# Optimization experiments

Measured on AMD Instinct MI355X. Metric: run time of the kernel, lower is better.

The kernel has to match this reference:

```python
import jax, jax.numpy as jnp
import numpy as np

D = 256      # model_dim
H = 4        # num_heads
DPH = D // H # dim_per_head = 64
NLBL = 9     # number of per-label linear layers


def setup_inputs() -> dict:
    key0 = jax.random.key(0)
    ks = jax.random.split(key0, 16)
    N, M = 6144, 6144
    s = 1.0 / np.sqrt(D)
    inp = {
        'key':     jax.random.normal(ks[0], (N, D), jnp.float32),
        'value':   jax.random.normal(ks[1], (N, D), jnp.float32),
        'query':   jax.random.normal(ks[2], (M, D), jnp.float32),
        'label_1': jax.random.randint(ks[3], (N,), 0, NLBL),
        'label_2': jax.random.randint(ks[4], (M,), 0, NLBL),
        # 9 per-label projection weights (applied as x @ W + b)
        'Wq': jax.random.normal(ks[5], (NLBL, D, D), jnp.float32) * s,
        'bq': jax.random.normal(ks[6], (NLBL, D), jnp.float32) * 0.02,
        'Wk': jax.random.normal(ks[7], (NLBL, D, D), jnp.float32) * s,
        'bk': jax.random.normal(ks[8], (NLBL, D), jnp.float32) * 0.02,
        'Wv': jax.random.normal(ks[9], (NLBL, D, D), jnp.float32) * s,
        'bv': jax.random.normal(ks[10], (NLBL, D), jnp.float32) * 0.02,
        'Wf': jax.random.normal(ks[11], (D, D), jnp.float32) * s,
        'bf': jax.random.normal(ks[12], (D,), jnp.float32) * 0.02,
        'gamma': jnp.ones((D,), jnp.float32),
        'beta':  jnp.zeros((D,), jnp.float32),
    }
    return inp


def _label_proj(x, W, b, lbl):
    # Project every token with all 9 label weights, then pick the per-token one.
    # p: [n, 9, D]
    p = jnp.einsum('nd,ldo->nlo', x, W) + b[None]
    return jnp.take_along_axis(p, lbl[:, None, None], axis=1)[:, 0]  # [n, D]


def reference(key, value, query, label_1, label_2,
              Wq, bq, Wk, bk, Wv, bv, Wf, bf, gamma, beta):
    M = query.shape[0]
    # Per-label (dynamically routed) projections; within a group the query
    # label equals the key label, so per-token weight selection is exactly
    # the per-group loop of the original module.
    q = _label_proj(query, Wq, bq, label_2).reshape(M, H, DPH)
    k = _label_proj(key,   Wk, bk, label_1).reshape(-1, H, DPH)
    v = _label_proj(value, Wv, bv, label_1).reshape(-1, H, DPH)

    # Note: original uses scale = (dim_per_head // num_heads) ** -0.5
    scale = (DPH // H) ** (-0.5)
    scores = jnp.einsum('mhd,nhd->hmn', q, k) * scale  # [H, M, N]

    # Queries only attend to keys of the same label (block structure of
    # the original per-label gather/attention/scatter loop).
    mask = label_2[:, None] == label_1[None, :]        # [M, N]
    probs = jax.nn.softmax(jnp.where(mask[None], scores, -1e30), axis=-1)

    ctx = jnp.einsum('hmn,nhd->mhd', probs, v).reshape(M, D)
    out = ctx @ Wf + bf
    res = query + out  # residual is the unprojected query

    mu = jnp.mean(res, axis=-1, keepdims=True)
    var = jnp.var(res, axis=-1, keepdims=True)
    return (res - mu) / jnp.sqrt(var + 1e-5) * gamma + beta
```

## Files before the change

kernel.cpp:

```cpp
#include <hip/hip_runtime.h>
#include <hip/hip_bf16.h>

#define D 256
#define H 4
#define DPH 64
#define NLBL 9
#define SPLITK 4

typedef __attribute__((ext_vector_type(8))) __bf16 bf16x8;
typedef __attribute__((ext_vector_type(8))) unsigned short u16x8;
typedef __attribute__((ext_vector_type(4))) float f32x4;

__device__ __forceinline__ int sw_idx(int row, int col) {
  return row * 64 + (col ^ ((row & 7) << 3));
}

__device__ __forceinline__ unsigned int pk2(float a, float b) {
  unsigned int lo = (unsigned int)__builtin_bit_cast(unsigned short, (__bf16)a);
  unsigned int hi = (unsigned int)__builtin_bit_cast(unsigned short, (__bf16)b);
  return lo | (hi << 16);
}

__device__ __forceinline__ bf16x8 cvt8(float4 u0, float4 u1) {
  bf16x8 r;
  r[0] = (__bf16)u0.x; r[1] = (__bf16)u0.y; r[2] = (__bf16)u0.z; r[3] = (__bf16)u0.w;
  r[4] = (__bf16)u1.x; r[5] = (__bf16)u1.y; r[6] = (__bf16)u1.z; r[7] = (__bf16)u1.w;
  return r;
}

__global__ __launch_bounds__(1024) void hist_kernel(
    const int* __restrict__ lbl1, int n1, const int* __restrict__ lbl2, int n2,
    int* __restrict__ cnt) {
  const int a = blockIdx.x;
  const int n = (a == 0) ? n1 : n2;
  const int* lbl = (a == 0) ? lbl1 : lbl2;
  const int t = threadIdx.x, lane = t & 63;

  __shared__ int bins[NLBL];
  if (t < NLBL) bins[t] = 0;
  __syncthreads();

  for (int chunk = 0; chunk < n; chunk += 1024) {
    int i = chunk + t;
    int l = (i < n) ? lbl[i] : -1;
#pragma unroll
    for (int lab = 0; lab < NLBL; ++lab) {
      unsigned long long bal = __ballot(l == lab);
      if (lane == 0 && bal) atomicAdd(&bins[lab], __popcll(bal));
    }
  }
  __syncthreads();
  if (t < NLBL) cnt[a * NLBL + t] = bins[t];
}

__global__ void offsets_kernel(const int* __restrict__ cnt, int* __restrict__ off,
                               int* __restrict__ pqo, int* __restrict__ pko,
                               int* __restrict__ tq, int* __restrict__ tk,
                               int* __restrict__ ntl) {
  if (threadIdx.x != 0) return;
  int a0 = 0, a1 = 0, p0 = 0, p1 = 0, t0 = 0, t1 = 0;
  for (int l = 0; l < NLBL; ++l) {
    off[l] = a0;      a0 += cnt[l];
    off[10 + l] = a1; a1 += cnt[NLBL + l];
    pko[l] = p0; pqo[l] = p1;
    int tkl = (cnt[l] + 63) >> 6, tql = (cnt[NLBL + l] + 63) >> 6;
    for (int i = 0; i < tkl; ++i) { tk[2 * t0] = l; tk[2 * t0 + 1] = p0 + (i << 6); ++t0; }
    for (int i = 0; i < tql; ++i) { tq[2 * t1] = l; tq[2 * t1 + 1] = p1 + (i << 6); ++t1; }
    p0 += tkl << 6; p1 += tql << 6;
  }
  off[9] = a0; off[19] = a1; pko[9] = p0; pqo[9] = p1;
  ntl[0] = t1; ntl[1] = t0;
}

__global__ __launch_bounds__(1024) void scatter_kernel(
    const int* __restrict__ lbl1, int n1, const int* __restrict__ lbl2, int n2,
    const int* __restrict__ off, int* __restrict__ korder, int* __restrict__ qorder) {
  const int l = blockIdx.x;
  const int a = blockIdx.y;
  const int n = (a == 0) ? n1 : n2;
  const int* lbl = (a == 0) ? lbl1 : lbl2;
  int* order = (a == 0) ? korder : qorder;
  const int base = off[a * 10 + l];

  const int t = threadIdx.x, wave = t >> 6, lane = t & 63;
  __shared__ int wtot[16];
  int pos = 0;
  for (int chunk = 0; chunk < n; chunk += 1024) {
    int i = chunk + t;
    bool flag = (i < n) && (lbl[i] == l);
    unsigned long long bal = __ballot(flag);
    int wprefix = __popcll(bal & ((1ull << lane) - 1ull));
    if (lane == 0) wtot[wave] = __popcll(bal);
    __syncthreads();
    int prew = 0, tot = 0;
#pragma unroll
    for (int w = 0; w < 16; ++w) {
      prew += (w < wave) ? wtot[w] : 0;
      tot += wtot[w];
    }
    if (flag) order[base + pos + prew + wprefix] = i;
    pos += tot;
    __syncthreads();
  }
}

__global__ __launch_bounds__(256) void transW_kernel(
    const float* __restrict__ Wq, const float* __restrict__ Wk,
    const float* __restrict__ Wv, const float* __restrict__ Wf,
    __bf16* __restrict__ Wqt, __bf16* __restrict__ Wkt,
    __bf16* __restrict__ Wvt, __bf16* __restrict__ Wft) {
  int m = blockIdx.y, sub = blockIdx.x;
  const float* src; __bf16* dst;
  if (m < 9)       { src = Wq + (size_t)m * 65536;        dst = Wqt + (size_t)m * 65536; }
  else if (m < 18) { src = Wk + (size_t)(m - 9) * 65536;  dst = Wkt + (size_t)(m - 9) * 65536; }
  else if (m < 27) { src = Wv + (size_t)(m - 18) * 65536; dst = Wvt + (size_t)(m - 18) * 65536; }
  else             { src = Wf;                            dst = Wft; }
  int k0 = (sub >> 2) << 6, n0 = (sub & 3) << 6;
  __shared__ float lds[64][65];
  int t = threadIdx.x, rr = t >> 6, c = t & 63;
#pragma unroll
  for (int i = 0; i < 16; ++i) {
    int r = i * 4 + rr;
    lds[r][c] = src[(size_t)(k0 + r) * D + n0 + c];
  }
  __syncthreads();
#pragma unroll
  for (int i = 0; i < 16; ++i) {
    int r = i * 4 + rr;
    dst[(size_t)(n0 + r) * D + k0 + c] = (__bf16)lds[c][r];
  }
}

__global__ __launch_bounds__(256) void gemm_in_kernel(
    const float* __restrict__ query, const float* __restrict__ key,
    const float* __restrict__ value,
    const __bf16* __restrict__ Wqt, const __bf16* __restrict__ Wkt,
    const __bf16* __restrict__ Wvt,
    const float* __restrict__ bq, const float* __restrict__ bk,
    const float* __restrict__ bv,
    const int* __restrict__ qorder, const int* __restrict__ korder,
    const int* __restrict__ off, const int* __restrict__ cnt,
    const int* __restrict__ pqo, const int* __restrict__ pko,
    const int* __restrict__ tq, const int* __restrict__ tk,
    const int* __restrict__ ntl,
    __bf16* __restrict__ qbuf, __bf16* __restrict__ kbuf, __bf16* __restrict__ vbuf) {
  const int y = blockIdx.y;
  const int nt = (y == 0) ? ntl[0] : ntl[1];
  const int ti = blockIdx.x >> 1, half = blockIdx.x & 1;
  if (ti >= nt) return;
  const int* tt = (y == 0) ? tq : tk;
  const float* x = (y == 0) ? query : (y == 1 ? key : value);
  const __bf16* W = (y == 0) ? Wqt : (y == 1 ? Wkt : Wvt);
  const float* bias = (y == 0) ? bq : (y == 1 ? bk : bv);
  const int* order = (y == 0) ? qorder : korder;
  const int* po = (y == 0) ? pqo : pko;
  __bf16* outp = (y == 0) ? qbuf : (y == 1 ? kbuf : vbuf);
  const float sc = (y == 0) ? 0.36067376f : 1.0f;

  const int l = tt[2 * ti], prow0 = tt[2 * ti + 1] + half * 32;
  const int cl = (y == 0) ? cnt[NLBL + l] : cnt[l];
  const int ooff = (y == 0) ? off[10 + l] : off[l];
  const int base = prow0 - po[l];

  const int t = threadIdx.x, w = t >> 6, lane = t & 63;
  const int lr = lane & 15, lk = lane >> 4;

  int src[2];
#pragma unroll
  for (int fi = 0; fi < 2; ++fi) {
    int ridx = base + fi * 16 + lr;
    src[fi] = (ridx < cl) ? order[ooff + ridx] : -1;
  }

  bf16x8 az;
#pragma unroll
  for (int j = 0; j < 8; ++j) az[j] = (__bf16)0.f;

  f32x4 acc[2][4];
#pragma unroll
  for (int i = 0; i < 2; ++i)
#pragma unroll
    for (int j = 0; j < 4; ++j) acc[i][j] = (f32x4){0.f, 0.f, 0.f, 0.f};

  for (int kb = 0; kb < 8; ++kb) {
    const int kbase = kb * 32 + lk * 8;
    bf16x8 a[2], b[4];
#pragma unroll
    for (int fi = 0; fi < 2; ++fi) {
      if (src[fi] >= 0) {
        const float* ap = x + (size_t)src[fi] * D + kbase;
        float4 u0 = *(const float4*)ap;
        float4 u1 = *(const float4*)(ap + 4);
        a[fi] = cvt8(u0, u1);
      } else {
        a[fi] = az;
      }
    }
#pragma unroll
    for (int fj = 0; fj < 4; ++fj) {
      int col = w * 64 + fj * 16 + lr;
      b[fj] = *(const bf16x8*)(W + (size_t)l * 65536 + (size_t)col * D + kbase);
    }
#pragma unroll
    for (int fi = 0; fi < 2; ++fi)
#pragma unroll
      for (int fj = 0; fj < 4; ++fj)
        acc[fi][fj] = __builtin_amdgcn_mfma_f32_16x16x32_bf16(a[fi], b[fj], acc[fi][fj], 0, 0, 0);
  }

#pragma unroll
  for (int fj = 0; fj < 4; ++fj) {
    int col = w * 64 + fj * 16 + lr;
    float bv_ = bias[l * D + col];
#pragma unroll
    for (int fi = 0; fi < 2; ++fi)
#pragma unroll
      for (int r = 0; r < 4; ++r) {
        int row = prow0 + fi * 16 + lk * 4 + r;
        outp[(size_t)row * D + col] = (__bf16)((acc[fi][fj][r] + bv_) * sc);
      }
  }
}

__global__ __launch_bounds__(256) void attn_mfma(
    const __bf16* __restrict__ qbuf, const __bf16* __restrict__ kbuf,
    const __bf16* __restrict__ vbuf, const int* __restrict__ cnt,
    const int* __restrict__ tq, const int* __restrict__ ntl,
    const int* __restrict__ pko,
    float* __restrict__ pctx, float* __restrict__ pstats) {
  const int tqi = blockIdx.x;
  if (tqi >= ntl[0]) return;
  const int l = tq[2 * tqi], prow0 = tq[2 * tqi + 1];
  const int h = blockIdx.y, s = blockIdx.z;
  const int nk = cnt[l];
  const int ntiles = (nk + 63) >> 6;
  const int ntsz = (ntiles + SPLITK - 1) / SPLITK;
  const int tt0 = s * ntsz;
  const int tt1 = min(ntiles, tt0 + ntsz);
  if (tt0 >= tt1) return;

  const int t = threadIdx.x;
  const int w = t >> 6, lane = t & 63;
  const int lr = lane & 15, lk = lane >> 4;

  __shared__ __align__(16) unsigned short ks[4096];
  __shared__ __align__(16) unsigned short vtl[4096];
  __shared__ __align__(16) unsigned short plds[4096];

  const int qloc = w * 16 + lr;
  const int qrow = prow0 + qloc;
  bf16x8 b_q[2];
#pragma unroll
  for (int kb = 0; kb < 2; ++kb)
    b_q[kb] = *(const bf16x8*)(qbuf + (size_t)qrow * D + h * DPH + kb * 32 + lk * 8);

  f32x4 acc_o[4];
#pragma unroll
  for (int i = 0; i < 4; ++i) acc_o[i] = (f32x4){0.f, 0.f, 0.f, 0.f};
  float mrun = -3.4e38f, lrun = 0.f;
  const int kb0 = pko[l];

  for (int tt = tt0; tt < tt1; ++tt) {
    const int n0 = tt << 6;
    __syncthreads();
    {
      int row = t >> 2, c0 = (t & 3) * 16;
      const uint4* kp = (const uint4*)(kbuf + (size_t)(kb0 + n0 + row) * D + h * DPH + c0);
      uint4 k0 = kp[0], k1 = kp[1];
      *(uint4*)&ks[sw_idx(row, c0)] = k0;
      *(uint4*)&ks[sw_idx(row, c0 + 8)] = k1;
    }
    {
      int key2 = (t & 31) * 2, d0 = (t >> 5) * 8;
      const unsigned short* vp = (const unsigned short*)(vbuf + (size_t)(kb0 + n0 + key2) * D + h * DPH + d0);
      u16x8 va = *(const u16x8*)vp;
      u16x8 vb = *(const u16x8*)(vp + D);
#pragma unroll
      for (int j = 0; j < 8; ++j) {
        unsigned int u = (unsigned int)va[j] | ((unsigned int)vb[j] << 16);
        *(unsigned int*)&vtl[sw_idx(d0 + j, key2)] = u;
      }
    }
    __syncthreads();

    f32x4 s_acc[4];
    const f32x4 zz = {0.f, 0.f, 0.f, 0.f};
#pragma unroll
    for (int fi = 0; fi < 4; ++fi) {
      bf16x8 a0 = *(const bf16x8*)&ks[sw_idx(fi * 16 + lr, lk * 8)];
      s_acc[fi] = __builtin_amdgcn_mfma_f32_16x16x32_bf16(a0, b_q[0], zz, 0, 0, 0);
    }
#pragma unroll
    for (int fi = 0; fi < 4; ++fi) {
      bf16x8 a1 = *(const bf16x8*)&ks[sw_idx(fi * 16 + lr, 32 + lk * 8)];
      s_acc[fi] = __builtin_amdgcn_mfma_f32_16x16x32_bf16(a1, b_q[1], s_acc[fi], 0, 0, 0);
    }

    float p[16];
    float tm = -3.4e38f;
#pragma unroll
    for (int fi = 0; fi < 4; ++fi)
#pragma unroll
      for (int r = 0; r < 4; ++r) {
        int key = n0 + fi * 16 + lk * 4 + r;
        float v = (key < nk) ? s_acc[fi][r] : -1e30f;
        p[fi * 4 + r] = v;
        tm = fmaxf(tm, v);
      }
    tm = fmaxf(tm, __shfl_xor(tm, 16, 64));
    tm = fmaxf(tm, __shfl_xor(tm, 32, 64));
    float mnew = fmaxf(mrun, tm);
    float alpha = exp2f(mrun - mnew);
    lrun *= alpha;
#pragma unroll
    for (int fi = 0; fi < 4; ++fi) acc_o[fi] = acc_o[fi] * alpha;
    float ts = 0.f;
#pragma unroll
    for (int i = 0; i < 16; ++i) { p[i] = exp2f(p[i] - mnew); ts += p[i]; }
    ts += __shfl_xor(ts, 16, 64);
    ts += __shfl_xor(ts, 32, 64);
    lrun += ts;
    mrun = mnew;

#pragma unroll
    for (int fi = 0; fi < 4; ++fi) {
      unsigned int w0 = pk2(p[fi * 4 + 0], p[fi * 4 + 1]);
      unsigned int w1 = pk2(p[fi * 4 + 2], p[fi * 4 + 3]);
      int idx = w * 1024 + sw_idx(lr, fi * 16 + lk * 4);
      *(uint2*)&plds[idx] = make_uint2(w0, w1);
    }

#pragma unroll
    for (int kb = 0; kb < 2; ++kb) {
      bf16x8 bp = *(const bf16x8*)&plds[w * 1024 + sw_idx(lr, kb * 32 + lk * 8)];
#pragma unroll
      for (int fi = 0; fi < 4; ++fi) {
        bf16x8 av = *(const bf16x8*)&vtl[sw_idx(fi * 16 + lr, kb * 32 + lk * 8)];
        acc_o[fi] = __builtin_amdgcn_mfma_f32_16x16x32_bf16(av, bp, acc_o[fi], 0, 0, 0);
      }
    }
  }

  const size_t base = ((size_t)tqi * H + h) * SPLITK + s;
  float* pc = pctx + base * 4096;
#pragma unroll
  for (int fi = 0; fi < 4; ++fi)
    *(f32x4*)(pc + qloc * 64 + fi * 16 + lk * 4) = acc_o[fi];
  if (lk == 0) {
    pstats[base * 128 + qloc * 2] = mrun;
    pstats[base * 128 + qloc * 2 + 1] = lrun;
  }
}

__global__ __launch_bounds__(256) void attn_reduce(
    const float* __restrict__ pctx, const float* __restrict__ pstats,
    const int* __restrict__ cnt, const int* __restrict__ tq,
    const int* __restrict__ ntl, __bf16* __restrict__ cg) {
  const int tqi = blockIdx.x;
  if (tqi >= ntl[0]) return;
  const int l = tq[2 * tqi], prow0 = tq[2 * tqi + 1];
  const int h = blockIdx.y;
  const int t = threadIdx.x;
  const int q = t >> 2, part = t & 3;

  __bf16* op = cg + (size_t)(prow0 + q) * D + h * DPH + part * 16;

  const int nk = cnt[l];
  const int ntiles = (nk + 63) >> 6;
  float o[16];
#pragma unroll
  for (int j = 0; j < 16; ++j) o[j] = 0.f;

  if (ntiles > 0) {
    const int ntsz = (ntiles + SPLITK - 1) / SPLITK;
    const int nsp = (ntiles + ntsz - 1) / ntsz;
    const size_t base0 = ((size_t)tqi * H + h) * SPLITK;

    float m = -3.4e38f;
    for (int s = 0; s < nsp; ++s)
      m = fmaxf(m, pstats[(base0 + s) * 128 + q * 2]);
    float L = 0.f;
    float wgt[SPLITK];
    for (int s = 0; s < nsp; ++s) {
      float ms = pstats[(base0 + s) * 128 + q * 2];
      float ls = pstats[(base0 + s) * 128 + q * 2 + 1];
      wgt[s] = exp2f(ms - m);
      L += ls * wgt[s];
    }
    float inv = (L > 0.f) ? (1.f / L) : 0.f;
    for (int s = 0; s < nsp; ++s) {
      const float* pc = pctx + (base0 + s) * 4096 + q * 64 + part * 16;
      float wg = wgt[s] * inv;
#pragma unroll
      for (int j = 0; j < 16; ++j) o[j] += pc[j] * wg;
    }
  }

  uint4 o0, o1;
  o0.x = pk2(o[0], o[1]);  o0.y = pk2(o[2], o[3]);
  o0.z = pk2(o[4], o[5]);  o0.w = pk2(o[6], o[7]);
  o1.x = pk2(o[8], o[9]);  o1.y = pk2(o[10], o[11]);
  o1.z = pk2(o[12], o[13]); o1.w = pk2(o[14], o[15]);
  *(uint4*)op = o0;
  *(uint4*)(op + 8) = o1;
}

__global__ __launch_bounds__(256) void proj_ln_kernel(
    const __bf16* __restrict__ cg, const __bf16* __restrict__ Wft,
    const float* __restrict__ bf_, const float* __restrict__ query,
    const int* __restrict__ qorder, const int* __restrict__ off,
    const int* __restrict__ cnt, const int* __restrict__ pqo,
    const int* __restrict__ tq, const int* __restrict__ ntl,
    const float* __restrict__ gamma, const float* __restrict__ beta,
    float* __restrict__ out) {
  const int tqi = blockIdx.x;
  if (tqi >= ntl[0]) return;
  const int l = tq[2 * tqi];
  const int prow0 = tq[2 * tqi + 1] + blockIdx.y * 32;
  const int cl = cnt[NLBL + l];
  const int ooff = off[10 + l];
  const int base = prow0 - pqo[l];

  const int t = threadIdx.x, w = t >> 6, lane = t & 63;
  const int lr = lane & 15, lk = lane >> 4;

  __shared__ int srcs[32];
  __shared__ float psum[4][32], psum2[4][32];
  __shared__ float mu_s[32], is_s[32];

  if (t < 32) {
    int ridx = base + t;
    srcs[t] = (ridx < cl) ? qorder[ooff + ridx] : -1;
  }

  f32x4 acc[2][4];
#pragma unroll
  for (int i = 0; i < 2; ++i)
#pragma unroll
    for (int j = 0; j < 4; ++j) acc[i][j] = (f32x4){0.f, 0.f, 0.f, 0.f};

  for (int kb = 0; kb < 8; ++kb) {
    const int kbase = kb * 32 + lk * 8;
    bf16x8 a[2], b[4];
#pragma unroll
    for (int fi = 0; fi < 2; ++fi)
      a[fi] = *(const bf16x8*)(cg + (size_t)(prow0 + fi * 16 + lr) * D + kbase);
#pragma unroll
    for (int fj = 0; fj < 4; ++fj) {
      int col = w * 64 + fj * 16 + lr;
      b[fj] = *(const bf16x8*)(Wft + (size_t)col * D + kbase);
    }
#pragma unroll
    for (int fi = 0; fi < 2; ++fi)
#pragma unroll
      for (int fj = 0; fj < 4; ++fj)
        acc[fi][fj] = __builtin_amdgcn_mfma_f32_16x16x32_bf16(a[fi], b[fj], acc[fi][fj], 0, 0, 0);
  }

  __syncthreads();

  float res[2][4][4];
  float s1[2][4], s2[2][4];
#pragma unroll
  for (int fi = 0; fi < 2; ++fi)
#pragma unroll
    for (int r = 0; r < 4; ++r) { s1[fi][r] = 0.f; s2[fi][r] = 0.f; }

#pragma unroll
  for (int fj = 0; fj < 4; ++fj) {
    int col = w * 64 + fj * 16 + lr;
    float bcol = bf_[col];
#pragma unroll
    for (int fi = 0; fi < 2; ++fi)
#pragma unroll
      for (int r = 0; r < 4; ++r) {
        int rowl = fi * 16 + lk * 4 + r;
        int sr = srcs[rowl];
        float qv = (sr >= 0) ? query[(size_t)sr * D + col] : 0.f;
        float v = acc[fi][fj][r] + bcol + qv;
        res[fi][fj][r] = v;
        s1[fi][r] += v;
        s2[fi][r] += v * v;
      }
  }

#pragma unroll
  for (int o2 = 1; o2 <= 8; o2 <<= 1) {
#pragma unroll
    for (int fi = 0; fi < 2; ++fi)
#pragma unroll
      for (int r = 0; r < 4; ++r) {
        s1[fi][r] += __shfl_xor(s1[fi][r], o2, 64);
        s2[fi][r] += __shfl_xor(s2[fi][r], o2, 64);
      }
  }
  if (lr == 0) {
#pragma unroll
    for (int fi = 0; fi < 2; ++fi)
#pragma unroll
      for (int r = 0; r < 4; ++r) {
        int rowl = fi * 16 + lk * 4 + r;
        psum[w][rowl] = s1[fi][r];
        psum2[w][rowl] = s2[fi][r];
      }
  }
  __syncthreads();
  if (t < 32) {
    float tot = psum[0][t] + psum[1][t] + psum[2][t] + psum[3][t];
    float tot2 = psum2[0][t] + psum2[1][t] + psum2[2][t] + psum2[3][t];
    float mu = tot * (1.f / D);
    float var = tot2 * (1.f / D) - mu * mu;
    mu_s[t] = mu;
    is_s[t] = rsqrtf(var + 1e-5f);
  }
  __syncthreads();

#pragma unroll
  for (int fj = 0; fj < 4; ++fj) {
    int col = w * 64 + fj * 16 + lr;
    float gc = gamma[col], bc = beta[col];
#pragma unroll
    for (int fi = 0; fi < 2; ++fi)
#pragma unroll
      for (int r = 0; r < 4; ++r) {
        int rowl = fi * 16 + lk * 4 + r;
        int sr = srcs[rowl];
        if (sr >= 0)
          out[(size_t)sr * D + col] =
              (res[fi][fj][r] - mu_s[rowl]) * is_s[rowl] * gc + bc;
      }
  }
}

extern "C" void kernel_launch(void* const* d_in, const int* in_sizes, int n_in,
                              void* d_out, int out_size, void* d_ws, size_t ws_size,
                              hipStream_t stream) {
  const float* key   = (const float*)d_in[0];
  const float* value = (const float*)d_in[1];
  const float* query = (const float*)d_in[2];
  const int*   lbl1  = (const int*)d_in[3];
  const int*   lbl2  = (const int*)d_in[4];
  const float* Wq = (const float*)d_in[5];
  const float* bq = (const float*)d_in[6];
  const float* Wk = (const float*)d_in[7];
  const float* bk = (const float*)d_in[8];
  const float* Wv = (const float*)d_in[9];
  const float* bv = (const float*)d_in[10];
  const float* Wf = (const float*)d_in[11];
  const float* bf_ = (const float*)d_in[12];
  const float* gamma = (const float*)d_in[13];
  const float* beta  = (const float*)d_in[14];
  float* out = (float*)d_out;

  const int N = in_sizes[0] / D;
  const int M = in_sizes[2] / D;
  const int MP = M + NLBL * 64;
  const int NP = N + NLBL * 64;
  const int TQCAP = (M + 63) / 64 + NLBL;
  const int TKCAP = (N + 63) / 64 + NLBL;

  int* cnt = (int*)d_ws;
  int* off = cnt + 32;
  int* pqo = off + 32;
  int* pko = pqo + 16;
  int* ntl = pko + 16;
  int* tq  = ntl + 16;
  int* tk  = tq + 2 * TQCAP;
  int* korder = tk + 2 * TKCAP;
  int* qorder = korder + N;
  size_t ihdr = (((size_t)(112 + 2 * TQCAP + 2 * TKCAP + N + M)) * 4 + 255) & ~(size_t)255;

  __bf16* Wqt = (__bf16*)((char*)d_ws + ihdr);
  __bf16* Wkt = Wqt + (size_t)9 * 65536;
  __bf16* Wvt = Wkt + (size_t)9 * 65536;
  __bf16* Wft = Wvt + (size_t)9 * 65536;
  __bf16* cg  = Wft + 65536;
  __bf16* qbuf = cg + (size_t)MP * D;
  __bf16* kbuf = qbuf + (size_t)MP * D;
  __bf16* vbuf = kbuf + (size_t)NP * D;
  float* pctx = (float*)(vbuf + (size_t)NP * D);
  float* pstats = pctx + (size_t)TQCAP * H * SPLITK * 4096;

  hist_kernel<<<2, 1024, 0, stream>>>(lbl1, N, lbl2, M, cnt);
  offsets_kernel<<<1, 1, 0, stream>>>(cnt, off, pqo, pko, tq, tk, ntl);
  dim3 sgrid(NLBL, 2);
  scatter_kernel<<<sgrid, 1024, 0, stream>>>(lbl1, N, lbl2, M, off, korder, qorder);

  transW_kernel<<<dim3(16, 28), 256, 0, stream>>>(Wq, Wk, Wv, Wf, Wqt, Wkt, Wvt, Wft);

  int gx = (TQCAP > TKCAP) ? TQCAP : TKCAP;
  gemm_in_kernel<<<dim3(gx * 2, 3), 256, 0, stream>>>(
      query, key, value, Wqt, Wkt, Wvt, bq, bk, bv,
      qorder, korder, off, cnt, pqo, pko, tq, tk, ntl, qbuf, kbuf, vbuf);

  attn_mfma<<<dim3(TQCAP, H, SPLITK), 256, 0, stream>>>(
      qbuf, kbuf, vbuf, cnt, tq, ntl, pko, pctx, pstats);

  attn_reduce<<<dim3(TQCAP, H), 256, 0, stream>>>(pctx, pstats, cnt, tq, ntl, cg);

  proj_ln_kernel<<<dim3(TQCAP, 2), 256, 0, stream>>>(
      cg, Wft, bf_, query, qorder, off, cnt, pqo, tq, ntl, gamma, beta, out);
}
```

Baseline: 104.9 us.

## Enlarge query tiles, drop running max, fuse split-K reduce into projection

Merges the histogram and offsets kernels into one single-block setup kernel. Query tiles grow to 128 rows so each attention wave processes two 16-row query fragments per K/V tile, doubling K/V reuse from LDS. The online-softmax running max and rescaling are removed and probabilities use exp2 of the raw scaled scores directly. The separate split-K reduce kernel is folded into proj_ln, which sums the partial contexts into LDS before the output GEMM. Skipping the max subtraction risks overflow for large scores, and the larger tiles reduce grid parallelism.

```diff
diff --git a/kernel.cpp b/kernel.cpp
--- a/kernel.cpp
+++ b/kernel.cpp
@@ -28,48 +28,45 @@
   return r;
 }
 
-__global__ __launch_bounds__(1024) void hist_kernel(
+__global__ __launch_bounds__(1024) void setup_kernel(
     const int* __restrict__ lbl1, int n1, const int* __restrict__ lbl2, int n2,
-    int* __restrict__ cnt) {
-  const int a = blockIdx.x;
-  const int n = (a == 0) ? n1 : n2;
-  const int* lbl = (a == 0) ? lbl1 : lbl2;
+    int* __restrict__ cnt, int* __restrict__ off,
+    int* __restrict__ pqo, int* __restrict__ pko,
+    int* __restrict__ tq, int* __restrict__ tk, int* __restrict__ ntl) {
   const int t = threadIdx.x, lane = t & 63;
-
-  __shared__ int bins[NLBL];
-  if (t < NLBL) bins[t] = 0;
-  __syncthreads();
-
-  for (int chunk = 0; chunk < n; chunk += 1024) {
-    int i = chunk + t;
-    int l = (i < n) ? lbl[i] : -1;
-#pragma unroll
-    for (int lab = 0; lab < NLBL; ++lab) {
-      unsigned long long bal = __ballot(l == lab);
-      if (lane == 0 && bal) atomicAdd(&bins[lab], __popcll(bal));
-    }
-  }
-  __syncthreads();
-  if (t < NLBL) cnt[a * NLBL + t] = bins[t];
-}
-
-__global__ void offsets_kernel(const int* __restrict__ cnt, int* __restrict__ off,
-                               int* __restrict__ pqo, int* __restrict__ pko,
-                               int* __restrict__ tq, int* __restrict__ tk,
-                               int* __restrict__ ntl) {
-  if (threadIdx.x != 0) return;
-  int a0 = 0, a1 = 0, p0 = 0, p1 = 0, t0 = 0, t1 = 0;
-  for (int l = 0; l < NLBL; ++l) {
-    off[l] = a0;      a0 += cnt[l];
-    off[10 + l] = a1; a1 += cnt[NLBL + l];
-    pko[l] = p0; pqo[l] = p1;
-    int tkl = (cnt[l] + 63) >> 6, tql = (cnt[NLBL + l] + 63) >> 6;
-    for (int i = 0; i < tkl; ++i) { tk[2 * t0] = l; tk[2 * t0 + 1] = p0 + (i << 6); ++t0; }
-    for (int i = 0; i < tql; ++i) { tq[2 * t1] = l; tq[2 * t1 + 1] = p1 + (i << 6); ++t1; }
-    p0 += tkl << 6; p1 += tql << 6;
-  }
-  off[9] = a0; off[19] = a1; pko[9] = p0; pqo[9] = p1;
-  ntl[0] = t1; ntl[1] = t0;
+  __shared__ int bins[2 * NLBL];
+  if (t < 2 * NLBL) bins[t] = 0;
+  __syncthreads();
+  for (int a = 0; a < 2; ++a) {
+    const int n = a ? n2 : n1;
+    const int* lbl = a ? lbl2 : lbl1;
+    for (int chunk = 0; chunk < n; chunk += 1024) {
+      int i = chunk + t;
+      int l = (i < n) ? lbl[i] : -1;
+#pragma unroll
+      for (int lab = 0; lab < NLBL; ++lab) {
+        unsigned long long bal = __ballot(l == lab);
+        if (lane == 0 && bal) atomicAdd(&bins[a * NLBL + lab], __popcll(bal));
+      }
+    }
+  }
+  __syncthreads();
+  if (t < 2 * NLBL) cnt[t] = bins[t];
+  if (t == 0) {
+    int a0 = 0, a1 = 0, p0 = 0, p1 = 0, t0 = 0, t1 = 0;
+    for (int l = 0; l < NLBL; ++l) {
+      off[l] = a0;      a0 += bins[l];
+      off[10 + l] = a1; a1 += bins[NLBL + l];
+      pko[l] = p0; pqo[l] = p1;
+      int tkl = (bins[l] + 63) >> 6;
+      int tql = (bins[NLBL + l] + 127) >> 7;
+      for (int i = 0; i < tkl; ++i) { tk[2 * t0] = l; tk[2 * t0 + 1] = p0 + (i << 6); ++t0; }
+      for (int i = 0; i < tql; ++i) { tq[2 * t1] = l; tq[2 * t1 + 1] = p1 + (i << 7); ++t1; }
+      p0 += tkl << 6; p1 += tql << 7;
+    }
+    off[9] = a0; off[19] = a1; pko[9] = p0; pqo[9] = p1;
+    ntl[0] = t1; ntl[1] = t0;
+  }
 }
 
 __global__ __launch_bounds__(1024) void scatter_kernel(
@@ -146,7 +143,8 @@
     __bf16* __restrict__ qbuf, __bf16* __restrict__ kbuf, __bf16* __restrict__ vbuf) {
   const int y = blockIdx.y;
   const int nt = (y == 0) ? ntl[0] : ntl[1];
-  const int ti = blockIdx.x >> 1, half = blockIdx.x & 1;
+  const int ti = (y == 0) ? ((int)blockIdx.x >> 2) : ((int)blockIdx.x >> 1);
+  const int sub = (y == 0) ? ((int)blockIdx.x & 3) : ((int)blockIdx.x & 1);
   if (ti >= nt) return;
   const int* tt = (y == 0) ? tq : tk;
   const float* x = (y == 0) ? query : (y == 1 ? key : value);
@@ -157,7 +155,7 @@
   __bf16* outp = (y == 0) ? qbuf : (y == 1 ? kbuf : vbuf);
   const float sc = (y == 0) ? 0.36067376f : 1.0f;
 
-  const int l = tt[2 * ti], prow0 = tt[2 * ti + 1] + half * 32;
+  const int l = tt[2 * ti], prow0 = tt[2 * ti + 1] + sub * 32;
   const int cl = (y == 0) ? cnt[NLBL + l] : cnt[l];
   const int ooff = (y == 0) ? off[10 + l] : off[l];
   const int base = prow0 - po[l];
@@ -245,19 +243,23 @@
 
   __shared__ __align__(16) unsigned short ks[4096];
   __shared__ __align__(16) unsigned short vtl[4096];
-  __shared__ __align__(16) unsigned short plds[4096];
-
-  const int qloc = w * 16 + lr;
-  const int qrow = prow0 + qloc;
-  bf16x8 b_q[2];
-#pragma unroll
-  for (int kb = 0; kb < 2; ++kb)
-    b_q[kb] = *(const bf16x8*)(qbuf + (size_t)qrow * D + h * DPH + kb * 32 + lk * 8);
-
-  f32x4 acc_o[4];
-#pragma unroll
-  for (int i = 0; i < 4; ++i) acc_o[i] = (f32x4){0.f, 0.f, 0.f, 0.f};
-  float mrun = -3.4e38f, lrun = 0.f;
+  __shared__ __align__(16) unsigned short plds[8192];
+
+  const int qbase = prow0 + w * 32;
+  bf16x8 b_q[2][2];
+#pragma unroll
+  for (int qf = 0; qf < 2; ++qf)
+#pragma unroll
+    for (int kb = 0; kb < 2; ++kb)
+      b_q[qf][kb] = *(const bf16x8*)(qbuf + (size_t)(qbase + qf * 16 + lr) * D +
+                                     h * DPH + kb * 32 + lk * 8);
+
+  f32x4 acc_o[2][4];
+#pragma unroll
+  for (int qf = 0; qf < 2; ++qf)
+#pragma unroll
+    for (int i = 0; i < 4; ++i) acc_o[qf][i] = (f32x4){0.f, 0.f, 0.f, 0.f};
+  float lrun[2] = {0.f, 0.f};
   const int kb0 = pko[l];
 
   for (int tt = tt0; tt < tt1; ++tt) {
@@ -283,131 +285,83 @@
     }
     __syncthreads();
 
-    f32x4 s_acc[4];
+    f32x4 s_acc[2][4];
     const f32x4 zz = {0.f, 0.f, 0.f, 0.f};
 #pragma unroll
     for (int fi = 0; fi < 4; ++fi) {
       bf16x8 a0 = *(const bf16x8*)&ks[sw_idx(fi * 16 + lr, lk * 8)];
-      s_acc[fi] = __builtin_amdgcn_mfma_f32_16x16x32_bf16(a0, b_q[0], zz, 0, 0, 0);
+#pragma unroll
+      for (int qf = 0; qf < 2; ++qf)
+        s_acc[qf][fi] = __builtin_amdgcn_mfma_f32_16x16x32_bf16(a0, b_q[qf][0], zz, 0, 0, 0);
     }
 #pragma unroll
     for (int fi = 0; fi < 4; ++fi) {
       bf16x8 a1 = *(const bf16x8*)&ks[sw_idx(fi * 16 + lr, 32 + lk * 8)];
-      s_acc[fi] = __builtin_amdgcn_mfma_f32_16x16x32_bf16(a1, b_q[1], s_acc[fi], 0, 0, 0);
-    }
-
-    float p[16];
-    float tm = -3.4e38f;
-#pragma unroll
-    for (int fi = 0; fi < 4; ++fi)
-#pragma unroll
-      for (int r = 0; r < 4; ++r) {
-        int key = n0 + fi * 16 + lk * 4 + r;
-        float v = (key < nk) ? s_acc[fi][r] : -1e30f;
-        p[fi * 4 + r] = v;
-        tm = fmaxf(tm, v);
-      }
-    tm = fmaxf(tm, __shfl_xor(tm, 16, 64));
-    tm = fmaxf(tm, __shfl_xor(tm, 32, 64));
-    float mnew = fmaxf(mrun, tm);
-    float alpha = exp2f(mrun - mnew);
-    lrun *= alpha;
-#pragma unroll
-    for (int fi = 0; fi < 4; ++fi) acc_o[fi] = acc_o[fi] * alpha;
-    float ts = 0.f;
-#pragma unroll
-    for (int i = 0; i < 16; ++i) { p[i] = exp2f(p[i] - mnew); ts += p[i]; }
-    ts += __shfl_xor(ts, 16, 64);
-    ts += __shfl_xor(ts, 32, 64);
-    lrun += ts;
-    mrun = mnew;
-
-#pragma unroll
-    for (int fi = 0; fi < 4; ++fi) {
-      unsigned int w0 = pk2(p[fi * 4 + 0], p[fi * 4 + 1]);
-      unsigned int w1 = pk2(p[fi * 4 + 2], p[fi * 4 + 3]);
-      int idx = w * 1024 + sw_idx(lr, fi * 16 + lk * 4);
-      *(uint2*)&plds[idx] = make_uint2(w0, w1);
-    }
+#pragma unroll
+      for (int qf = 0; qf < 2; ++qf)
+        s_acc[qf][fi] = __builtin_amdgcn_mfma_f32_16x16x32_bf16(a1, b_q[qf][1], s_acc[qf][fi], 0, 0, 0);
+    }
+
+    float p[2][16];
+#pragma unroll
+    for (int qf = 0; qf < 2; ++qf) {
+      float ts = 0.f;
+#pragma unroll
+      for (int fi = 0; fi < 4; ++fi)
+#pragma unroll
+        for (int r = 0; r < 4; ++r) {
+          int key = n0 + fi * 16 + lk * 4 + r;
+          float pv = (key < nk) ? exp2f(s_acc[qf][fi][r]) : 0.f;
+          p[qf][fi * 4 + r] = pv;
+          ts += pv;
+        }
+      ts += __shfl_xor(ts, 16, 64);
+      ts += __shfl_xor(ts, 32, 64);
+      lrun[qf] += ts;
+    }
+
+#pragma unroll
+    for (int qf = 0; qf < 2; ++qf)
+#pragma unroll
+      for (int fi = 0; fi < 4; ++fi) {
+        unsigned int w0 = pk2(p[qf][fi * 4 + 0], p[qf][fi * 4 + 1]);
+        unsigned int w1 = pk2(p[qf][fi * 4 + 2], p[qf][fi * 4 + 3]);
+        int idx = w * 2048 + sw_idx(qf * 16 + lr, fi * 16 + lk * 4);
+        *(uint2*)&plds[idx] = make_uint2(w0, w1);
+      }
 
 #pragma unroll
     for (int kb = 0; kb < 2; ++kb) {
-      bf16x8 bp = *(const bf16x8*)&plds[w * 1024 + sw_idx(lr, kb * 32 + lk * 8)];
+      bf16x8 bp[2];
+#pragma unroll
+      for (int qf = 0; qf < 2; ++qf)
+        bp[qf] = *(const bf16x8*)&plds[w * 2048 + sw_idx(qf * 16 + lr, kb * 32 + lk * 8)];
 #pragma unroll
       for (int fi = 0; fi < 4; ++fi) {
         bf16x8 av = *(const bf16x8*)&vtl[sw_idx(fi * 16 + lr, kb * 32 + lk * 8)];
-        acc_o[fi] = __builtin_amdgcn_mfma_f32_16x16x32_bf16(av, bp, acc_o[fi], 0, 0, 0);
-      }
-    }
-  }
-
-  const size_t base = ((size_t)tqi * H + h) * SPLITK + s;
-  float* pc = pctx + base * 4096;
-#pragma unroll
-  for (int fi = 0; fi < 4; ++fi)
-    *(f32x4*)(pc + qloc * 64 + fi * 16 + lk * 4) = acc_o[fi];
-  if (lk == 0) {
-    pstats[base * 128 + qloc * 2] = mrun;
-    pstats[base * 128 + qloc * 2 + 1] = lrun;
-  }
-}
-
-__global__ __launch_bounds__(256) void attn_reduce(
+#pragma unroll
+        for (int qf = 0; qf < 2; ++qf)
+          acc_o[qf][fi] = __builtin_amdgcn_mfma_f32_16x16x32_bf16(av, bp[qf], acc_o[qf][fi], 0, 0, 0);
+      }
+    }
+  }
+
+  const size_t pbase = ((size_t)tqi * H + h) * SPLITK + s;
+  float* pc = pctx + pbase * 8192;
+#pragma unroll
+  for (int qf = 0; qf < 2; ++qf) {
+    int qloc = w * 32 + qf * 16 + lr;
+#pragma unroll
+    for (int fi = 0; fi < 4; ++fi)
+      *(f32x4*)(pc + qloc * 64 + fi * 16 + lk * 4) = acc_o[qf][fi];
+    if (lk == 0) pstats[pbase * 128 + qloc] = lrun[qf];
+  }
+}
+
+__global__ __launch_bounds__(256) void proj_ln_kernel(
     const float* __restrict__ pctx, const float* __restrict__ pstats,
-    const int* __restrict__ cnt, const int* __restrict__ tq,
-    const int* __restrict__ ntl, __bf16* __restrict__ cg) {
-  const int tqi = blockIdx.x;
-  if (tqi >= ntl[0]) return;
-  const int l = tq[2 * tqi], prow0 = tq[2 * tqi + 1];
-  const int h = blockIdx.y;
-  const int t = threadIdx.x;
-  const int q = t >> 2, part = t & 3;
-
-  __bf16* op = cg + (size_t)(prow0 + q) * D + h * DPH + part * 16;
-
-  const int nk = cnt[l];
-  const int ntiles = (nk + 63) >> 6;
-  float o[16];
-#pragma unroll
-  for (int j = 0; j < 16; ++j) o[j] = 0.f;
-
-  if (ntiles > 0) {
-    const int ntsz = (ntiles + SPLITK - 1) / SPLITK;
-    const int nsp = (ntiles + ntsz - 1) / ntsz;
-    const size_t base0 = ((size_t)tqi * H + h) * SPLITK;
-
-    float m = -3.4e38f;
-    for (int s = 0; s < nsp; ++s)
-      m = fmaxf(m, pstats[(base0 + s) * 128 + q * 2]);
-    float L = 0.f;
-    float wgt[SPLITK];
-    for (int s = 0; s < nsp; ++s) {
-      float ms = pstats[(base0 + s) * 128 + q * 2];
-      float ls = pstats[(base0 + s) * 128 + q * 2 + 1];
-      wgt[s] = exp2f(ms - m);
-      L += ls * wgt[s];
-    }
-    float inv = (L > 0.f) ? (1.f / L) : 0.f;
-    for (int s = 0; s < nsp; ++s) {
-      const float* pc = pctx + (base0 + s) * 4096 + q * 64 + part * 16;
-      float wg = wgt[s] * inv;
-#pragma unroll
-      for (int j = 0; j < 16; ++j) o[j] += pc[j] * wg;
-    }
-  }
-
-  uint4 o0, o1;
-  o0.x = pk2(o[0], o[1]);  o0.y = pk2(o[2], o[3]);
-  o0.z = pk2(o[4], o[5]);  o0.w = pk2(o[6], o[7]);
-  o1.x = pk2(o[8], o[9]);  o1.y = pk2(o[10], o[11]);
-  o1.z = pk2(o[12], o[13]); o1.w = pk2(o[14], o[15]);
-  *(uint4*)op = o0;
-  *(uint4*)(op + 8) = o1;
-}
-
-__global__ __launch_bounds__(256) void proj_ln_kernel(
-    const __bf16* __restrict__ cg, const __bf16* __restrict__ Wft,
-    const float* __restrict__ bf_, const float* __restrict__ query,
+    const __bf16* __restrict__ Wft, const float* __restrict__ bf_,
+    const float* __restrict__ query,
     const int* __restrict__ qorder, const int* __restrict__ off,
     const int* __restrict__ cnt, const int* __restrict__ pqo,
     const int* __restrict__ tq, const int* __restrict__ ntl,
@@ -416,15 +370,23 @@
   const int tqi = blockIdx.x;
   if (tqi >= ntl[0]) return;
   const int l = tq[2 * tqi];
-  const int prow0 = tq[2 * tqi + 1] + blockIdx.y * 32;
+  const int qq = blockIdx.y;
+  const int prow0 = tq[2 * tqi + 1] + qq * 32;
+  const int qloc0 = qq * 32;
   const int cl = cnt[NLBL + l];
   const int ooff = off[10 + l];
   const int base = prow0 - pqo[l];
+  const int nk = cnt[l];
+  const int ntiles = (nk + 63) >> 6;
+  const int ntsz = (ntiles + SPLITK - 1) / SPLITK;
+  const int nsp = ntiles ? (ntiles + ntsz - 1) / ntsz : 0;
 
   const int t = threadIdx.x, w = t >> 6, lane = t & 63;
   const int lr = lane & 15, lk = lane >> 4;
 
   __shared__ int srcs[32];
+  __shared__ float linv[32][4];
+  __shared__ __align__(16) unsigned short ct[32 * 256];
   __shared__ float psum[4][32], psum2[4][32];
   __shared__ float mu_s[32], is_s[32];
 
@@ -432,6 +394,38 @@
     int ridx = base + t;
     srcs[t] = (ridx < cl) ? qorder[ooff + ridx] : -1;
   }
+  if (t < 128) {
+    int row = t >> 2, h = t & 3;
+    float L = 0.f;
+    for (int s = 0; s < nsp; ++s)
+      L += pstats[(((size_t)tqi * H + h) * SPLITK + s) * 128 + qloc0 + row];
+    linv[row][h] = (L > 0.f) ? (1.f / L) : 0.f;
+  }
+  __syncthreads();
+
+  {
+    int row = t >> 3, dseg = (t & 7) * 32;
+    int h = dseg >> 6, d0 = dseg & 63;
+    const float* pb = pctx + (((size_t)tqi * H + h) * SPLITK) * 8192 +
+                      (size_t)(qloc0 + row) * 64 + d0;
+    float v[32];
+#pragma unroll
+    for (int j = 0; j < 32; ++j) v[j] = 0.f;
+    for (int s = 0; s < nsp; ++s) {
+      const float* ps = pb + (size_t)s * 8192;
+#pragma unroll
+      for (int j = 0; j < 32; j += 4) {
+        f32x4 u = *(const f32x4*)(ps + j);
+        v[j] += u[0]; v[j + 1] += u[1]; v[j + 2] += u[2]; v[j + 3] += u[3];
+      }
+    }
+    float iv = linv[row][h];
+    int xr = (row & 7) << 3;
+#pragma unroll
+    for (int j = 0; j < 32; j += 2)
+      *(unsigned int*)&ct[row * 256 + ((dseg + j) ^ xr)] = pk2(v[j] * iv, v[j + 1] * iv);
+  }
+  __syncthreads();
 
   f32x4 acc[2][4];
 #pragma unroll
@@ -443,8 +437,10 @@
     const int kbase = kb * 32 + lk * 8;
     bf16x8 a[2], b[4];
 #pragma unroll
-    for (int fi = 0; fi < 2; ++fi)
-      a[fi] = *(const bf16x8*)(cg + (size_t)(prow0 + fi * 16 + lr) * D + kbase);
+    for (int fi = 0; fi < 2; ++fi) {
+      int row = fi * 16 + lr;
+      a[fi] = *(const bf16x8*)&ct[row * 256 + (kbase ^ ((row & 7) << 3))];
+    }
 #pragma unroll
     for (int fj = 0; fj < 4; ++fj) {
       int col = w * 64 + fj * 16 + lr;
@@ -456,8 +452,6 @@
       for (int fj = 0; fj < 4; ++fj)
         acc[fi][fj] = __builtin_amdgcn_mfma_f32_16x16x32_bf16(a[fi], b[fj], acc[fi][fj], 0, 0, 0);
   }
-
-  __syncthreads();
 
   float res[2][4][4];
   float s1[2][4], s2[2][4];
@@ -554,9 +548,9 @@
 
   const int N = in_sizes[0] / D;
   const int M = in_sizes[2] / D;
-  const int MP = M + NLBL * 64;
+  const int MP = M + NLBL * 128;
   const int NP = N + NLBL * 64;
-  const int TQCAP = (M + 63) / 64 + NLBL;
+  const int TQCAP = (M + 127) / 128 + NLBL;
   const int TKCAP = (N + 63) / 64 + NLBL;
 
   int* cnt = (int*)d_ws;
@@ -574,30 +568,28 @@
   __bf16* Wkt = Wqt + (size_t)9 * 65536;
   __bf16* Wvt = Wkt + (size_t)9 * 65536;
   __bf16* Wft = Wvt + (size_t)9 * 65536;
-  __bf16* cg  = Wft + 65536;
-  __bf16* qbuf = cg + (size_t)MP * D;
+  __bf16* qbuf = Wft + 65536;
   __bf16* kbuf = qbuf + (size_t)MP * D;
   __bf16* vbuf = kbuf + (size_t)NP * D;
   float* pctx = (float*)(vbuf + (size_t)NP * D);
-  float* pstats = pctx + (size_t)TQCAP * H * SPLITK * 4096;
-
-  hist_kernel<<<2, 1024, 0, stream>>>(lbl1, N, lbl2, M, cnt);
-  offsets_kernel<<<1, 1, 0, stream>>>(cnt, off, pqo, pko, tq, tk, ntl);
+  float* pstats = pctx + (size_t)TQCAP * H * SPLITK * 8192;
+
+  setup_kernel<<<1, 1024, 0, stream>>>(lbl1, N, lbl2, M, cnt, off, pqo, pko, tq, tk, ntl);
+
   dim3 sgrid(NLBL, 2);
   scatter_kernel<<<sgrid, 1024, 0, stream>>>(lbl1, N, lbl2, M, off, korder, qorder);
 
   transW_kernel<<<dim3(16, 28), 256, 0, stream>>>(Wq, Wk, Wv, Wf, Wqt, Wkt, Wvt, Wft);
 
-  int gx = (TQCAP > TKCAP) ? TQCAP : TKCAP;
-  gemm_in_kernel<<<dim3(gx * 2, 3), 256, 0, stream>>>(
+  int gx = TQCAP * 4 > TKCAP * 2 ? TQCAP * 4 : TKCAP * 2;
+  gemm_in_kernel<<<dim3(gx, 3), 256, 0, stream>>>(
       query, key, value, Wqt, Wkt, Wvt, bq, bk, bv,
       qorder, korder, off, cnt, pqo, pko, tq, tk, ntl, qbuf, kbuf, vbuf);
 
   attn_mfma<<<dim3(TQCAP, H, SPLITK), 256, 0, stream>>>(
       qbuf, kbuf, vbuf, cnt, tq, ntl, pko, pctx, pstats);
 
-  attn_reduce<<<dim3(TQCAP, H), 256, 0, stream>>>(pctx, pstats, cnt, tq, ntl, cg);
-
-  proj_ln_kernel<<<dim3(TQCAP, 2), 256, 0, stream>>>(
-      cg, Wft, bf_, query, qorder, off, cnt, pqo, tq, ntl, gamma, beta, out);
-}
+  proj_ln_kernel<<<dim3(TQCAP, 4), 256, 0, stream>>>(
+      pctx, pstats, Wft, bf_, query, qorder, off, cnt, pqo, tq, ntl,
+      gamma, beta, out);
+}
```

Result: no change. 105.3 us (+0.4%).
